# Kernel optimization log

Measured on AMD Instinct MI355X. Metric: run time of the kernel, lower is better.

The kernel has to match this reference:

```python
import jax, jax.numpy as jnp
import numpy as np

N, S, IN_F, TEXT_D, EMB, H = 128, 1024, 768, 512, 512, 8
HD = EMB // H  # 64


def setup_inputs() -> dict:
    key = jax.random.key(0)
    ks = jax.random.split(key, 14)
    sc = 0.02
    return {
        "v": jax.random.normal(ks[0], (1, N, 12, IN_F), dtype=jnp.float32),
        "t": jax.random.normal(ks[1], (N, S, TEXT_D), dtype=jnp.float32),
        "t_len": jax.random.randint(ks[2], (N,), 1, S + 1, dtype=jnp.int32),
        "W_fc1": jax.random.normal(ks[3], (EMB, IN_F), dtype=jnp.float32) * sc,
        "b_fc1": jnp.zeros((EMB,), jnp.float32),
        "W_fc2": jax.random.normal(ks[4], (EMB, 12 * EMB), dtype=jnp.float32) * sc,
        "b_fc2": jnp.zeros((EMB,), jnp.float32),
        "Wq": jax.random.normal(ks[5], (EMB, EMB), dtype=jnp.float32) * sc,
        "Wk": jax.random.normal(ks[6], (EMB, TEXT_D), dtype=jnp.float32) * sc,
        "Wv": jax.random.normal(ks[7], (EMB, TEXT_D), dtype=jnp.float32) * sc,
        "bq": jnp.zeros((EMB,), jnp.float32),
        "bk": jnp.zeros((EMB,), jnp.float32),
        "bv": jnp.zeros((EMB,), jnp.float32),
        "Wo": jax.random.normal(ks[8], (EMB, EMB), dtype=jnp.float32) * sc,
        "bo": jnp.zeros((EMB,), jnp.float32),
    }


def reference(v, t, t_len, W_fc1, b_fc1, W_fc2, b_fc2, Wq, Wk, Wv, bq, bk, bv, Wo, bo):
    # fc1 + ReLU: [1,N,12,IN_F] -> [N,12,EMB]
    x = jax.nn.relu(jnp.einsum('onif,ef->onie', v, W_fc1) + b_fc1)[0]
    # flatten + fc2 + ReLU -> [N, EMB]
    x = x.reshape(N, 12 * EMB)
    vfeat = jax.nn.relu(x @ W_fc2.T + b_fc2)
    # Batched ragged multihead attention, query length 1 per item.
    scale = 1.0 / jnp.sqrt(jnp.asarray(HD, vfeat.dtype))
    q = ((vfeat @ Wq.T + bq) * scale).reshape(N, H, HD)           # [N,H,HD]
    k = (jnp.einsum('nsd,ed->nse', t, Wk) + bk).reshape(N, S, H, HD)
    vv = (jnp.einsum('nsd,ed->nse', t, Wv) + bv).reshape(N, S, H, HD)
    scores = jnp.einsum('nhd,nshd->nhs', q, k)                    # [N,H,S]
    valid = (jnp.arange(S)[None, :] < t_len[:, None])[:, None, :]  # [N,1,S]
    scores = jnp.where(valid, scores, jnp.finfo(scores.dtype).min)
    w = jax.nn.softmax(scores, axis=-1)                           # [N,H,S]
    ctx = jnp.einsum('nhs,nshd->nhd', w, vv).reshape(N, EMB)
    attn_out = ctx @ Wo.T + bo                                    # [N,EMB]
    return vfeat, attn_out
```

## Files before the change

kernel.cpp:

```cpp
#include <hip/hip_runtime.h>

#define NB 128
#define SSEQ 1024
#define TD 512
#define TSTR 516

typedef _Float16 half8 __attribute__((ext_vector_type(8)));
typedef _Float16 half4 __attribute__((ext_vector_type(4)));
typedef float f32x4 __attribute__((ext_vector_type(4)));

template<int AM, int BM>
__device__ __forceinline__ void gemm_body(
    const void* __restrict__ Av, int lda, long aSZ,
    const void* __restrict__ Bv, int ldb, long bSZ,
    const float* __restrict__ bias, const float* __restrict__ biasS,
    const float* __restrict__ aRowScale,
    float scale, int doRelu, int outMode,
    float* __restrict__ outF, _Float16* __restrict__ outH,
    int ldc, int cColOff, int kTiles, long oSplit,
    int mt, int nt, int sp, int bz, int tid)
{
  __shared__ _Float16 As[64][72];
  __shared__ _Float16 Bs[64][72];
  int r = tid >> 2, kq = (tid & 3) * 16;
  int w = tid >> 6, l = tid & 63;
  long aoff = (long)bz * aSZ + (long)(mt * 64 + r) * lda + (long)sp * kTiles * 64 + kq;
  long boff = (long)bz * bSZ + (long)(nt * 64 + r) * ldb + (long)sp * kTiles * 64 + kq;
  const _Float16* apH = (const _Float16*)Av + aoff;
  const float*    apF = (const float*)Av + aoff;
  const _Float16* bpH = (const _Float16*)Bv + boff;
  const float*    bpF = (const float*)Bv + boff;
  float srA = 1.0f;
  if constexpr (AM == 2) srA = 1.0f / aRowScale[(mt * 64 + r) * 8 + sp];

  half8 pa0, pa1, pb0, pb1;
  f32x4 qa0, qa1, qa2, qa3, qc0, qc1, qc2, qc3;
  if constexpr (AM == 0) { pa0 = *(const half8*)apH; pa1 = *(const half8*)(apH + 8); }
  else { qa0 = *(const f32x4*)apF; qa1 = *(const f32x4*)(apF + 4);
         qa2 = *(const f32x4*)(apF + 8); qa3 = *(const f32x4*)(apF + 12); }
  if constexpr (BM == 0) { pb0 = *(const half8*)bpH; pb1 = *(const half8*)(bpH + 8); }
  else { qc0 = *(const f32x4*)bpF; qc1 = *(const f32x4*)(bpF + 4);
         qc2 = *(const f32x4*)(bpF + 8); qc3 = *(const f32x4*)(bpF + 12); }

  f32x4 acc[4];
  #pragma unroll
  for (int c = 0; c < 4; ++c) acc[c] = (f32x4){0.f, 0.f, 0.f, 0.f};
  int fr = l & 15, fo = (l >> 4) * 8;
  for (int kt = 0; kt < kTiles; ++kt) {
    __syncthreads();
    if constexpr (AM == 0) {
      *(half8*)&As[r][kq] = pa0; *(half8*)&As[r][kq + 8] = pa1;
    } else {
      f32x4 s0 = qa0, s1 = qa1, s2 = qa2, s3 = qa3;
      if constexpr (AM == 2) { s0 *= srA; s1 *= srA; s2 *= srA; s3 *= srA; }
      *(half4*)&As[r][kq + 0]  = __builtin_convertvector(s0, half4);
      *(half4*)&As[r][kq + 4]  = __builtin_convertvector(s1, half4);
      *(half4*)&As[r][kq + 8]  = __builtin_convertvector(s2, half4);
      *(half4*)&As[r][kq + 12] = __builtin_convertvector(s3, half4);
    }
    if constexpr (BM == 0) {
      *(half8*)&Bs[r][kq] = pb0; *(half8*)&Bs[r][kq + 8] = pb1;
    } else {
      *(half4*)&Bs[r][kq + 0]  = __builtin_convertvector(qc0, half4);
      *(half4*)&Bs[r][kq + 4]  = __builtin_convertvector(qc1, half4);
      *(half4*)&Bs[r][kq + 8]  = __builtin_convertvector(qc2, half4);
      *(half4*)&Bs[r][kq + 12] = __builtin_convertvector(qc3, half4);
    }
    __syncthreads();
    if (kt + 1 < kTiles) {
      apH += 64; apF += 64; bpH += 64; bpF += 64;
      if constexpr (AM == 0) { pa0 = *(const half8*)apH; pa1 = *(const half8*)(apH + 8); }
      else { qa0 = *(const f32x4*)apF; qa1 = *(const f32x4*)(apF + 4);
             qa2 = *(const f32x4*)(apF + 8); qa3 = *(const f32x4*)(apF + 12); }
      if constexpr (BM == 0) { pb0 = *(const half8*)bpH; pb1 = *(const half8*)(bpH + 8); }
      else { qc0 = *(const f32x4*)bpF; qc1 = *(const f32x4*)(bpF + 4);
             qc2 = *(const f32x4*)(bpF + 8); qc3 = *(const f32x4*)(bpF + 12); }
    }
    #pragma unroll
    for (int ks = 0; ks < 2; ++ks) {
      half8 af = *(const half8*)&As[16 * w + fr][ks * 32 + fo];
      #pragma unroll
      for (int c = 0; c < 4; ++c) {
        half8 bf = *(const half8*)&Bs[16 * c + fr][ks * 32 + fo];
        acc[c] = __builtin_amdgcn_mfma_f32_16x16x32_f16(af, bf, acc[c], 0, 0, 0);
      }
    }
  }
  int lrow = (l >> 4) * 4, lcol = l & 15;
  #pragma unroll
  for (int c = 0; c < 4; ++c) {
    #pragma unroll
    for (int rr = 0; rr < 4; ++rr) {
      int gm = mt * 64 + 16 * w + lrow + rr;
      int gn = nt * 64 + 16 * c + lcol;
      int ecol = gn + bz * cColOff;
      float vv = acc[c][rr];
      if (bias && sp == 0) vv += bias[ecol];
      if (biasS) vv += biasS[sp * 512 + ecol];
      vv *= scale;
      if (doRelu) vv = fmaxf(vv, 0.f);
      long oidx = (long)gm * ldc + ecol;
      if (outMode == 0) outF[oidx] = vv;
      else if (outMode == 1) outH[oidx] = (_Float16)vv;
      else if (outMode == 2) outF[oidx + (long)sp * oSplit] = vv;
      else atomicAdd(&outF[oidx], vv);
    }
  }
}

template<int AM, int BM>
__global__ __launch_bounds__(256) void k_gemm(
    const void* __restrict__ Av, int lda, long aSZ,
    const void* __restrict__ Bv, int ldb, long bSZ,
    const float* __restrict__ bias, const float* __restrict__ biasS,
    const float* __restrict__ aRowScale,
    float scale, int doRelu, int outMode,
    float* __restrict__ outF, _Float16* __restrict__ outH,
    int ldc, int cColOff, int mtiles, int kTiles, long oSplit)
{
  gemm_body<AM, BM>(Av, lda, aSZ, Bv, ldb, bSZ, bias, biasS, aRowScale, scale, doRelu,
                    outMode, outF, outH, ldc, cColOff, kTiles, oSplit,
                    (int)blockIdx.x % mtiles, (int)blockIdx.x / mtiles,
                    (int)blockIdx.y, (int)blockIdx.z, (int)threadIdx.x);
}

__global__ __launch_bounds__(256) void k_prepfc1(
    const float* __restrict__ Wq, const float* __restrict__ Wk,
    const float* __restrict__ bq, const float* __restrict__ bk,
    _Float16* __restrict__ G16T, float* __restrict__ gb,
    float* __restrict__ qbc, float* __restrict__ cvec,
    float* __restrict__ pz, _Float16* __restrict__ qz,
    const float* __restrict__ v, const float* __restrict__ W1,
    const float* __restrict__ b1, _Float16* __restrict__ x16)
{
  int bx = blockIdx.x, tid = threadIdx.x;
  if (bx >= 512) {
    int s = bx - 512;
    gemm_body<1, 1>(v, 768, 0, W1, 768, 0, b1, nullptr, nullptr, 1.f, 1, 1,
                    nullptr, x16, 512, 0, 12, 0, s % 24, s / 24, 0, 0, tid);
    return;
  }
  int b = bx;
  int gid = b * 256 + tid;
  for (long i = gid; i < 131328; i += 131072)
    *(f32x4*)(pz + 4 * i) = (f32x4){0.f, 0.f, 0.f, 0.f};
  {
    long i4 = (long)gid * 4;
    long n = i4 >> 12, off = i4 & 4095;
    *(half4*)(qz + n * 8192 + 4096 + off) = (half4){(_Float16)0, (_Float16)0, (_Float16)0, (_Float16)0};
  }
  __shared__ float SA[64][68];
  __shared__ float SB[64][68];
  __shared__ float sv0[64], sv1[64];
  int r = tid >> 2, cq = (tid & 3) * 16;
  int te = tid & 15, td = tid >> 4;
  int h = b >> 6, et = (b >> 3) & 7, dt = b & 7;
  const float* wqp = Wq + (long)(h * 64 + r) * 512 + et * 64 + cq;
  const float* wkp = Wk + (long)(h * 64 + r) * 512 + dt * 64 + cq;
  #pragma unroll
  for (int c = 0; c < 4; ++c) {
    *(f32x4*)&SA[r][cq + 4 * c] = *(const f32x4*)(wqp + 4 * c);
    *(f32x4*)&SB[r][cq + 4 * c] = *(const f32x4*)(wkp + 4 * c);
  }
  if (tid < 64) { sv0[tid] = bq[h * 64 + tid]; sv1[tid] = bk[h * 64 + tid]; }
  __syncthreads();
  float acc[4][4];
  #pragma unroll
  for (int a = 0; a < 4; ++a)
    #pragma unroll
    for (int d = 0; d < 4; ++d) acc[a][d] = 0.f;
  #pragma unroll 4
  for (int j = 0; j < 64; ++j) {
    f32x4 av = *(const f32x4*)&SA[j][te * 4];
    f32x4 bv4 = *(const f32x4*)&SB[j][td * 4];
    #pragma unroll
    for (int a = 0; a < 4; ++a)
      #pragma unroll
      for (int d = 0; d < 4; ++d) acc[a][d] = fmaf(av[a], bv4[d], acc[a][d]);
  }
  #pragma unroll
  for (int d = 0; d < 4; ++d) {
    half4 hv = { (_Float16)(0.125f * acc[0][d]), (_Float16)(0.125f * acc[1][d]),
                 (_Float16)(0.125f * acc[2][d]), (_Float16)(0.125f * acc[3][d]) };
    *(half4*)(G16T + (long)h * 262144 + (long)(dt * 64 + td * 4 + d) * 512 + et * 64 + te * 4) = hv;
  }
  if (dt == 0 && td == 0) {
    #pragma unroll
    for (int i = 0; i < 4; ++i) {
      float s = 0.f;
      for (int j = 0; j < 64; ++j) s = fmaf(SA[j][te * 4 + i], sv1[j], s);
      gb[h * 512 + et * 64 + te * 4 + i] = 0.125f * s;
    }
  }
  if (et == 0 && te == 0) {
    #pragma unroll
    for (int i = 0; i < 4; ++i) {
      float s = 0.f;
      for (int j = 0; j < 64; ++j) s = fmaf(SB[j][td * 4 + i], sv0[j], s);
      cvec[h * 512 + dt * 64 + td * 4 + i] = 0.125f * s;
    }
  }
  if (et == 0 && dt == 0 && tid == 0) {
    float s = 0.f;
    for (int j = 0; j < 64; ++j) s = fmaf(sv0[j], sv1[j], s);
    qbc[h] = 0.125f * s;
  }
}

__global__ __launch_bounds__(256) void k_vfeat(
    const float* __restrict__ vacc, const float* __restrict__ b2,
    float* __restrict__ outF, _Float16* __restrict__ vf16,
    const float* __restrict__ Wv, const float* __restrict__ Wo,
    const float* __restrict__ bv, _Float16* __restrict__ M16,
    float* __restrict__ obo8)
{
  int bx = blockIdx.x, tid = threadIdx.x;
  __shared__ float SA[64][68];
  __shared__ float SB[64][68];
  __shared__ float sv0[64];
  if (bx < 256) {
    int i = bx * 256 + tid;
    float vv = b2[i & 511];
    #pragma unroll
    for (int sp = 0; sp < 16; ++sp) vv += vacc[sp * 65536 + i];
    vv = fmaxf(vv, 0.f);
    outF[i] = vv;
    vf16[i] = (_Float16)vv;
    return;
  }
  int b2i = bx - 256;
  int h = b2i >> 6, et = (b2i >> 3) & 7, gt = b2i & 7;
  int r = tid >> 2, cq = (tid & 3) * 16;
  int te = tid & 15, td = tid >> 4;
  const float* wvp = Wv + (long)(h * 64 + r) * 512 + gt * 64 + cq;
  const float* wop = Wo + (long)(et * 64 + r) * 512 + h * 64 + cq;
  #pragma unroll
  for (int c = 0; c < 4; ++c)
    *(f32x4*)&SA[r][cq + 4 * c] = *(const f32x4*)(wvp + 4 * c);
  #pragma unroll
  for (int c = 0; c < 4; ++c) {
    f32x4 x = *(const f32x4*)(wop + 4 * c);
    #pragma unroll
    for (int i = 0; i < 4; ++i) SB[cq + 4 * c + i][r] = x[i];
  }
  if (tid < 64) sv0[tid] = bv[h * 64 + tid];
  __syncthreads();
  float acc[4][4];
  #pragma unroll
  for (int a = 0; a < 4; ++a)
    #pragma unroll
    for (int d = 0; d < 4; ++d) acc[a][d] = 0.f;
  #pragma unroll 4
  for (int jj = 0; jj < 64; ++jj) {
    f32x4 av = *(const f32x4*)&SA[jj][te * 4];
    f32x4 bt = *(const f32x4*)&SB[jj][td * 4];
    #pragma unroll
    for (int a = 0; a < 4; ++a)
      #pragma unroll
      for (int d = 0; d < 4; ++d) acc[a][d] = fmaf(av[a], bt[d], acc[a][d]);
  }
  #pragma unroll
  for (int d = 0; d < 4; ++d) {
    half4 hv = { (_Float16)acc[0][d], (_Float16)acc[1][d],
                 (_Float16)acc[2][d], (_Float16)acc[3][d] };
    *(half4*)(M16 + (long)(et * 64 + td * 4 + d) * 4096 + h * 512 + gt * 64 + te * 4) = hv;
  }
  if (gt == 0 && te == 0) {
    float s0 = 0.f, s1 = 0.f, s2 = 0.f, s3 = 0.f;
    for (int jj = 0; jj < 64; ++jj) {
      f32x4 bt = *(const f32x4*)&SB[jj][td * 4];
      float bb = sv0[jj];
      s0 = fmaf(bt[0], bb, s0); s1 = fmaf(bt[1], bb, s1);
      s2 = fmaf(bt[2], bb, s2); s3 = fmaf(bt[3], bb, s3);
    }
    obo8[h * 512 + et * 64 + td * 4 + 0] = s0;
    obo8[h * 512 + et * 64 + td * 4 + 1] = s1;
    obo8[h * 512 + et * 64 + td * 4 + 2] = s2;
    obo8[h * 512 + et * 64 + td * 4 + 3] = s3;
  }
}

__global__ __launch_bounds__(256) void k_qkqb(
    const _Float16* __restrict__ vf16, const _Float16* __restrict__ G16T,
    const float* __restrict__ cvec, const float* __restrict__ gb,
    const float* __restrict__ qbc, _Float16* __restrict__ qk16,
    float* __restrict__ qb, float* __restrict__ outz)
{
  int bx = blockIdx.x, tid = threadIdx.x;
  if (bx < 128) {
    int z = bx >> 4, s = bx & 15;
    gemm_body<0, 0>(vf16, 512, 0, G16T, 512, 262144, cvec, nullptr, nullptr, 1.f, 0, 1,
                    nullptr, qk16, 8192, 512, 8, 0, s % 2, s / 2, 0, z, tid);
    return;
  }
  int n = bx - 128;
  float* oz = outz + (long)n * 512;
  oz[tid] = 0.f; oz[tid + 256] = 0.f;
  __shared__ float qs[512];
  qs[tid] = (float)vf16[n * 512 + tid];
  qs[tid + 256] = (float)vf16[n * 512 + tid + 256];
  __syncthreads();
  int h = tid >> 5, j = tid & 31;
  float p = 0.f;
  for (int e = j; e < 512; e += 32) p = fmaf(qs[e], gb[h * 512 + e], p);
  #pragma unroll
  for (int m = 1; m < 32; m <<= 1) p += __shfl_xor(p, m, 32);
  if (j == 0) qb[n * 8 + h] = p + qbc[h];
}

__global__ __launch_bounds__(256) void k_attn(
    const float* __restrict__ t, const int* __restrict__ tlen,
    const _Float16* __restrict__ qk16, const float* __restrict__ qb,
    float* __restrict__ pu, float* __restrict__ pl)
{
  int n = blockIdx.x >> 2, g = blockIdx.x & 3;
  int len = tlen[n];
  if (g * 256 >= len) return;
  int tid = threadIdx.x, wid = tid >> 6, l = tid & 63;
  int fr = l & 15, fo = (l >> 4) * 8;

  __shared__ __align__(16) _Float16 ts[64][TSTR];
  __shared__ __align__(16) _Float16 wst[16][72];

  const float* tn = t + (long)n * SSEQ * TD;
  const _Float16* qn = qk16 + (long)n * 8192 + fr * 512 + fo;
  float qbr = (fr < 8) ? qb[n * 8 + fr] : 0.f;

  f32x4 upv[8];
  #pragma unroll
  for (int dt = 0; dt < 8; ++dt) upv[dt] = (f32x4){0.f, 0.f, 0.f, 0.f};
  float lsum = 0.f;

  for (int jj = 0; jj < 4; ++jj) {
    int base = g * 256 + jj * 64;
    if (base >= len) break;
    int s1 = base + 64; if (s1 > len) s1 = len;
    if (jj) __syncthreads();
    {
      f32x4 a0, a1, b0, b1;
      auto ld = [&](int rr, f32x4& x0, f32x4& x1) {
        int sg = base + 16 * wid + rr;
        if (sg < s1) {
          const float* p = tn + (long)sg * TD;
          x0 = *(const f32x4*)(p + 4 * l);
          x1 = *(const f32x4*)(p + 256 + 4 * l);
        } else {
          x0 = (f32x4){0.f,0.f,0.f,0.f}; x1 = (f32x4){0.f,0.f,0.f,0.f};
        }
      };
      ld(0, a0, a1); ld(1, b0, b1);
      #pragma unroll
      for (int rr = 0; rr < 16; rr += 2) {
        half4 h0 = __builtin_convertvector(a0, half4);
        half4 h1 = __builtin_convertvector(a1, half4);
        int row = 16 * wid + rr;
        if (rr + 2 < 16) ld(rr + 2, a0, a1);
        *(half4*)&ts[row][4 * l] = h0;
        *(half4*)&ts[row][256 + 4 * l] = h1;
        half4 g0 = __builtin_convertvector(b0, half4);
        half4 g1 = __builtin_convertvector(b1, half4);
        if (rr + 3 < 16) ld(rr + 3, b0, b1);
        *(half4*)&ts[row + 1][4 * l] = g0;
        *(half4*)&ts[row + 1][256 + 4 * l] = g1;
      }
    }
    {
      f32x4 acc = (f32x4){0.f, 0.f, 0.f, 0.f};
      __builtin_amdgcn_s_setprio(1);
      #pragma unroll 4
      for (int kt = 0; kt < 16; ++kt) {
        half8 bf = *(const half8*)(qn + kt * 32);
        const _Float16* ap = &ts[16 * wid + fr][kt * 32 + fo];
        half4 alo = *(const half4*)ap;
        half4 ahi = *(const half4*)(ap + 4);
        half8 af = { alo[0], alo[1], alo[2], alo[3], ahi[0], ahi[1], ahi[2], ahi[3] };
        acc = __builtin_amdgcn_mfma_f32_16x16x32_f16(af, bf, acc, 0, 0, 0);
      }
      __builtin_amdgcn_s_setprio(0);
      #pragma unroll
      for (int r = 0; r < 4; ++r) {
        int sl = 16 * wid + (l >> 4) * 4 + r;
        float wv = (fr < 8 && base + sl < s1) ? __expf(acc[r] + qbr) : 0.f;
        wst[fr][sl] = (_Float16)wv;
        lsum += wv;
      }
    }
    __syncthreads();
    __builtin_amdgcn_s_setprio(1);
    #pragma unroll
    for (int dt = 0; dt < 8; ++dt) {
      int dcol = 128 * wid + dt * 16 + fr;
      #pragma unroll
      for (int ks = 0; ks < 2; ++ks) {
        half8 af = *(const half8*)&wst[fr][ks * 32 + fo];
        half8 bf;
        #pragma unroll
        for (int jx = 0; jx < 8; ++jx) bf[jx] = ts[ks * 32 + fo + jx][dcol];
        upv[dt] = __builtin_amdgcn_mfma_f32_16x16x32_f16(af, bf, upv[dt], 0, 0, 0);
      }
    }
    __builtin_amdgcn_s_setprio(0);
  }
  int quad = l >> 4;
  float* pn = pu + (long)n * 4096;
  if (quad < 2) {
    #pragma unroll
    for (int dt = 0; dt < 8; ++dt) {
      int d = 128 * wid + dt * 16 + fr;
      #pragma unroll
      for (int r = 0; r < 4; ++r)
        atomicAdd(&pn[(quad * 4 + r) * 512 + d], upv[dt][r]);
    }
  }
  if (fr < 8) atomicAdd(&pl[n * 8 + fr], lsum);
}

extern "C" void kernel_launch(void* const* d_in, const int* in_sizes, int n_in,
                              void* d_out, int out_size, void* d_ws, size_t ws_size,
                              hipStream_t stream)
{
  const float* v    = (const float*)d_in[0];
  const float* t    = (const float*)d_in[1];
  const int*   tlen = (const int*)d_in[2];
  const float* W1   = (const float*)d_in[3];
  const float* b1   = (const float*)d_in[4];
  const float* W2   = (const float*)d_in[5];
  const float* b2   = (const float*)d_in[6];
  const float* Wq   = (const float*)d_in[7];
  const float* Wk   = (const float*)d_in[8];
  const float* Wv   = (const float*)d_in[9];
  const float* bq   = (const float*)d_in[10];
  const float* bk   = (const float*)d_in[11];
  const float* bv   = (const float*)d_in[12];
  const float* Wo   = (const float*)d_in[13];
  const float* bo   = (const float*)d_in[14];
  float* out = (float*)d_out;

  _Float16* hb   = (_Float16*)d_ws;
  _Float16* x16  = hb;
  _Float16* vf16 = hb + 786432l;
  _Float16* qk16 = hb + 851968l;
  _Float16* G16T = hb + 1900544l;
  _Float16* M16  = hb + 3997696l;
  float* fb   = (float*)(hb + 6094848l);
  float* vacc = fb;
  float* pu   = fb + 1048576l;
  float* pl   = fb + 1572864l;
  float* qb   = fb + 1573888l;
  float* gb   = fb + 1574912l;
  float* qbc  = fb + 1579008l;
  float* cvec = fb + 1579024l;
  float* obo8 = fb + 1583120l;

  k_prepfc1<<<704, 256, 0, stream>>>(Wq, Wk, bq, bk, G16T, gb, qbc, cvec,
                                     pu, qk16, v, W1, b1, x16);
  k_gemm<0,1><<<dim3(16, 16, 1), 256, 0, stream>>>(x16, 6144, 0, W2, 6144, 0,
      nullptr, nullptr, nullptr, 1.f, 0, 2, vacc, nullptr, 512, 0, 2, 6, 65536);
  k_vfeat<<<768, 256, 0, stream>>>(vacc, b2, out, vf16, Wv, Wo, bv, M16, obo8);
  k_qkqb<<<256, 256, 0, stream>>>(vf16, G16T, cvec, gb, qbc, qk16, qb, out + 65536);
  k_attn<<<NB * 4, 256, 0, stream>>>(t, tlen, qk16, qb, pu, pl);
  k_gemm<2,0><<<dim3(16, 8, 1), 256, 0, stream>>>(pu, 4096, 0, M16, 4096, 0,
      bo, obo8, pl, 1.f, 0, 3, out + 65536, nullptr, 512, 0, 2, 8, 0);
}
```

Before: 455.5 us.

## Merge vfeat reduction into fc2 atomics, fuse kernels, interleave attention chunks

The fc2 GEMM now accumulates split-K partials directly into a zeroed fp32 buffer with atomics and bias, instead of writing 16 partial slices that a separate kernel reduces. ReLU and the fp16 conversion move into the A-load of the q·K GEMM, so the vfeat and qkqb kernels merge into one launch, using a shared-memory buffer passed into gemm_body. Attention now interleaves 64-row chunks across the four blocks per item, which balances work under ragged lengths. The cost is atomic contention and nondeterministic summation order in fc2.

Result: slower. 465.2 us (+2.1%).

```diff
diff --git a/kernel.cpp b/kernel.cpp
--- a/kernel.cpp
+++ b/kernel.cpp
@@ -11,6 +11,7 @@
 
 template<int AM, int BM>
 __device__ __forceinline__ void gemm_body(
+    char* smem,
     const void* __restrict__ Av, int lda, long aSZ,
     const void* __restrict__ Bv, int ldb, long bSZ,
     const float* __restrict__ bias, const float* __restrict__ biasS,
@@ -20,8 +21,8 @@
     int ldc, int cColOff, int kTiles, long oSplit,
     int mt, int nt, int sp, int bz, int tid)
 {
-  __shared__ _Float16 As[64][72];
-  __shared__ _Float16 Bs[64][72];
+  _Float16 (*As)[72] = (_Float16 (*)[72])smem;
+  _Float16 (*Bs)[72] = (_Float16 (*)[72])(smem + 9216);
   int r = tid >> 2, kq = (tid & 3) * 16;
   int w = tid >> 6, l = tid & 63;
   long aoff = (long)bz * aSZ + (long)(mt * 64 + r) * lda + (long)sp * kTiles * 64 + kq;
@@ -53,6 +54,13 @@
     } else {
       f32x4 s0 = qa0, s1 = qa1, s2 = qa2, s3 = qa3;
       if constexpr (AM == 2) { s0 *= srA; s1 *= srA; s2 *= srA; s3 *= srA; }
+      if constexpr (AM == 3) {
+        #pragma unroll
+        for (int ii = 0; ii < 4; ++ii) {
+          s0[ii] = fmaxf(s0[ii], 0.f); s1[ii] = fmaxf(s1[ii], 0.f);
+          s2[ii] = fmaxf(s2[ii], 0.f); s3[ii] = fmaxf(s3[ii], 0.f);
+        }
+      }
       *(half4*)&As[r][kq + 0]  = __builtin_convertvector(s0, half4);
       *(half4*)&As[r][kq + 4]  = __builtin_convertvector(s1, half4);
       *(half4*)&As[r][kq + 8]  = __builtin_convertvector(s2, half4);
@@ -118,7 +126,8 @@
     float* __restrict__ outF, _Float16* __restrict__ outH,
     int ldc, int cColOff, int mtiles, int kTiles, long oSplit)
 {
-  gemm_body<AM, BM>(Av, lda, aSZ, Bv, ldb, bSZ, bias, biasS, aRowScale, scale, doRelu,
+  __shared__ __align__(16) char sm[18432];
+  gemm_body<AM, BM>(sm, Av, lda, aSZ, Bv, ldb, bSZ, bias, biasS, aRowScale, scale, doRelu,
                     outMode, outF, outH, ldc, cColOff, kTiles, oSplit,
                     (int)blockIdx.x % mtiles, (int)blockIdx.x / mtiles,
                     (int)blockIdx.y, (int)blockIdx.z, (int)threadIdx.x);
@@ -133,25 +142,27 @@
     const float* __restrict__ v, const float* __restrict__ W1,
     const float* __restrict__ b1, _Float16* __restrict__ x16)
 {
+  __shared__ __align__(16) char sm[35328];
   int bx = blockIdx.x, tid = threadIdx.x;
   if (bx >= 512) {
     int s = bx - 512;
-    gemm_body<1, 1>(v, 768, 0, W1, 768, 0, b1, nullptr, nullptr, 1.f, 1, 1,
+    gemm_body<1, 1>(sm, v, 768, 0, W1, 768, 0, b1, nullptr, nullptr, 1.f, 1, 1,
                     nullptr, x16, 512, 0, 12, 0, s % 24, s / 24, 0, 0, tid);
     return;
   }
   int b = bx;
   int gid = b * 256 + tid;
-  for (long i = gid; i < 131328; i += 131072)
+  for (long i = gid; i < 147712; i += 131072)
     *(f32x4*)(pz + 4 * i) = (f32x4){0.f, 0.f, 0.f, 0.f};
   {
     long i4 = (long)gid * 4;
     long n = i4 >> 12, off = i4 & 4095;
     *(half4*)(qz + n * 8192 + 4096 + off) = (half4){(_Float16)0, (_Float16)0, (_Float16)0, (_Float16)0};
   }
-  __shared__ float SA[64][68];
-  __shared__ float SB[64][68];
-  __shared__ float sv0[64], sv1[64];
+  float (*SA)[68] = (float (*)[68])sm;
+  float (*SB)[68] = (float (*)[68])(sm + 17408);
+  float* sv0 = (float*)(sm + 34816);
+  float* sv1 = (float*)(sm + 35072);
   int r = tid >> 2, cq = (tid & 3) * 16;
   int te = tid & 15, td = tid >> 4;
   int h = b >> 6, et = (b >> 3) & 7, dt = b & 7;
@@ -207,29 +218,47 @@
   }
 }
 
-__global__ __launch_bounds__(256) void k_vfeat(
-    const float* __restrict__ vacc, const float* __restrict__ b2,
-    float* __restrict__ outF, _Float16* __restrict__ vf16,
+__global__ __launch_bounds__(256) void k_qkqb(
+    const float* __restrict__ vsum, const _Float16* __restrict__ G16T,
+    const float* __restrict__ cvec, const float* __restrict__ gb,
+    const float* __restrict__ qbc, _Float16* __restrict__ qk16,
+    float* __restrict__ qb, float* __restrict__ outz, float* __restrict__ out0,
     const float* __restrict__ Wv, const float* __restrict__ Wo,
     const float* __restrict__ bv, _Float16* __restrict__ M16,
     float* __restrict__ obo8)
 {
+  __shared__ __align__(16) char sm[35328];
   int bx = blockIdx.x, tid = threadIdx.x;
-  __shared__ float SA[64][68];
-  __shared__ float SB[64][68];
-  __shared__ float sv0[64];
+  if (bx < 128) {
+    int z = bx >> 4, s = bx & 15;
+    gemm_body<3, 0>(sm, vsum, 512, 0, G16T, 512, 262144, cvec, nullptr, nullptr, 1.f, 0, 1,
+                    nullptr, qk16, 8192, 512, 8, 0, s % 2, s / 2, 0, z, tid);
+    return;
+  }
   if (bx < 256) {
-    int i = bx * 256 + tid;
-    float vv = b2[i & 511];
-    #pragma unroll
-    for (int sp = 0; sp < 16; ++sp) vv += vacc[sp * 65536 + i];
-    vv = fmaxf(vv, 0.f);
-    outF[i] = vv;
-    vf16[i] = (_Float16)vv;
+    int n = bx - 128;
+    float* oz = outz + (long)n * 512;
+    oz[tid] = 0.f; oz[tid + 256] = 0.f;
+    float* qs = (float*)sm;
+    float v0 = fmaxf(vsum[n * 512 + tid], 0.f);
+    float v1 = fmaxf(vsum[n * 512 + tid + 256], 0.f);
+    out0[n * 512 + tid] = v0;
+    out0[n * 512 + tid + 256] = v1;
+    qs[tid] = v0; qs[tid + 256] = v1;
+    __syncthreads();
+    int h = tid >> 5, j = tid & 31;
+    float p = 0.f;
+    for (int e = j; e < 512; e += 32) p = fmaf(qs[e], gb[h * 512 + e], p);
+    #pragma unroll
+    for (int m = 1; m < 32; m <<= 1) p += __shfl_xor(p, m, 32);
+    if (j == 0) qb[n * 8 + h] = p + qbc[h];
     return;
   }
   int b2i = bx - 256;
   int h = b2i >> 6, et = (b2i >> 3) & 7, gt = b2i & 7;
+  float (*SA)[68] = (float (*)[68])sm;
+  float (*SB)[68] = (float (*)[68])(sm + 17408);
+  float* sv0 = (float*)(sm + 34816);
   int r = tid >> 2, cq = (tid & 3) * 16;
   int te = tid & 15, td = tid >> 4;
   const float* wvp = Wv + (long)(h * 64 + r) * 512 + gt * 64 + cq;
@@ -280,34 +309,6 @@
   }
 }
 
-__global__ __launch_bounds__(256) void k_qkqb(
-    const _Float16* __restrict__ vf16, const _Float16* __restrict__ G16T,
-    const float* __restrict__ cvec, const float* __restrict__ gb,
-    const float* __restrict__ qbc, _Float16* __restrict__ qk16,
-    float* __restrict__ qb, float* __restrict__ outz)
-{
-  int bx = blockIdx.x, tid = threadIdx.x;
-  if (bx < 128) {
-    int z = bx >> 4, s = bx & 15;
-    gemm_body<0, 0>(vf16, 512, 0, G16T, 512, 262144, cvec, nullptr, nullptr, 1.f, 0, 1,
-                    nullptr, qk16, 8192, 512, 8, 0, s % 2, s / 2, 0, z, tid);
-    return;
-  }
-  int n = bx - 128;
-  float* oz = outz + (long)n * 512;
-  oz[tid] = 0.f; oz[tid + 256] = 0.f;
-  __shared__ float qs[512];
-  qs[tid] = (float)vf16[n * 512 + tid];
-  qs[tid + 256] = (float)vf16[n * 512 + tid + 256];
-  __syncthreads();
-  int h = tid >> 5, j = tid & 31;
-  float p = 0.f;
-  for (int e = j; e < 512; e += 32) p = fmaf(qs[e], gb[h * 512 + e], p);
-  #pragma unroll
-  for (int m = 1; m < 32; m <<= 1) p += __shfl_xor(p, m, 32);
-  if (j == 0) qb[n * 8 + h] = p + qbc[h];
-}
-
 __global__ __launch_bounds__(256) void k_attn(
     const float* __restrict__ t, const int* __restrict__ tlen,
     const _Float16* __restrict__ qk16, const float* __restrict__ qb,
@@ -315,7 +316,7 @@
 {
   int n = blockIdx.x >> 2, g = blockIdx.x & 3;
   int len = tlen[n];
-  if (g * 256 >= len) return;
+  if (g * 64 >= len) return;
   int tid = threadIdx.x, wid = tid >> 6, l = tid & 63;
   int fr = l & 15, fo = (l >> 4) * 8;
 
@@ -332,7 +333,7 @@
   float lsum = 0.f;
 
   for (int jj = 0; jj < 4; ++jj) {
-    int base = g * 256 + jj * 64;
+    int base = (g + 4 * jj) * 64;
     if (base >= len) break;
     int s1 = base + 64; if (s1 > len) s1 = len;
     if (jj) __syncthreads();
@@ -438,26 +439,25 @@
 
   _Float16* hb   = (_Float16*)d_ws;
   _Float16* x16  = hb;
-  _Float16* vf16 = hb + 786432l;
-  _Float16* qk16 = hb + 851968l;
-  _Float16* G16T = hb + 1900544l;
-  _Float16* M16  = hb + 3997696l;
-  float* fb   = (float*)(hb + 6094848l);
-  float* vacc = fb;
-  float* pu   = fb + 1048576l;
-  float* pl   = fb + 1572864l;
-  float* qb   = fb + 1573888l;
-  float* gb   = fb + 1574912l;
-  float* qbc  = fb + 1579008l;
-  float* cvec = fb + 1579024l;
-  float* obo8 = fb + 1583120l;
+  _Float16* qk16 = hb + 786432l;
+  _Float16* G16T = hb + 1835008l;
+  _Float16* M16  = hb + 3932160l;
+  float* fb   = (float*)(hb + 6029312l);
+  float* vsum = fb;
+  float* pu   = fb + 65536l;
+  float* pl   = fb + 589824l;
+  float* qb   = fb + 590848l;
+  float* gb   = fb + 591872l;
+  float* qbc  = fb + 595968l;
+  float* cvec = fb + 595984l;
+  float* obo8 = fb + 600080l;
 
   k_prepfc1<<<704, 256, 0, stream>>>(Wq, Wk, bq, bk, G16T, gb, qbc, cvec,
-                                     pu, qk16, v, W1, b1, x16);
-  k_gemm<0,1><<<dim3(16, 16, 1), 256, 0, stream>>>(x16, 6144, 0, W2, 6144, 0,
-      nullptr, nullptr, nullptr, 1.f, 0, 2, vacc, nullptr, 512, 0, 2, 6, 65536);
-  k_vfeat<<<768, 256, 0, stream>>>(vacc, b2, out, vf16, Wv, Wo, bv, M16, obo8);
-  k_qkqb<<<256, 256, 0, stream>>>(vf16, G16T, cvec, gb, qbc, qk16, qb, out + 65536);
+                                     fb, qk16, v, W1, b1, x16);
+  k_gemm<0,1><<<dim3(16, 8, 1), 256, 0, stream>>>(x16, 6144, 0, W2, 6144, 0,
+      b2, nullptr, nullptr, 1.f, 0, 3, vsum, nullptr, 512, 0, 2, 12, 0);
+  k_qkqb<<<768, 256, 0, stream>>>(vsum, G16T, cvec, gb, qbc, qk16, qb,
+                                  out + 65536, out, Wv, Wo, bv, M16, obo8);
   k_attn<<<NB * 4, 256, 0, stream>>>(t, tlen, qk16, qb, pu, pl);
   k_gemm<2,0><<<dim3(16, 8, 1), 256, 0, stream>>>(pu, 4096, 0, M16, 4096, 0,
       bo, obo8, pl, 1.f, 0, 3, out + 65536, nullptr, 512, 0, 2, 8, 0);
```
